# Optimization experiments

Measured on AMD Instinct MI355X. Metric: run time of the kernel, lower is better.

## Reference

```python
import jax, jax.numpy as jnp
import numpy as np

NU, NS, NV = 50000, 10000, 30000
D = 128
NUM_LAYERS = 2
EPS_US, EPS_UV, EPS_SV = 0.1, 0.1, 0.1
C_TEMP = 0.2
B = 2048


def _l2(x, eps=1e-12):
    n = jnp.sqrt(jnp.sum(x * x, axis=-1, keepdims=True))
    return x / jnp.maximum(n, eps)


def _spmm(row, col, val, x, n_out):
    # COO sparse @ dense: gather rows of x, scale, segment-reduce
    return jax.ops.segment_sum(val[:, None] * x[col], row, num_segments=n_out)


def _propagate(row, col, val, a, b, eps, key):
    feats = jnp.concatenate([a, b], axis=0)
    n = feats.shape[0]
    acc = feats  # layer-0 features are NOT normalized in the original
    for i in range(NUM_LAYERS):
        feats = _spmm(row, col, val, feats, n)
        noise = jax.random.uniform(jax.random.fold_in(key, i), feats.shape, feats.dtype)
        feats = feats + jnp.sign(feats) * _l2(noise) * eps
        acc = acc + _l2(feats)
    mean = acc / (NUM_LAYERS + 1)
    return mean[: a.shape[0]], mean[a.shape[0]:]


def _aggregate(row, col, val, x, n_out, eps, key):
    agg = _spmm(row, col, val, x, n_out)
    noise = jax.random.uniform(key, agg.shape, agg.dtype)
    return agg + jnp.sign(agg) * _l2(noise) * eps


def _mga(users_list, streamers_list, lin_w, lin_b):
    embs = [jnp.concatenate([u, s], axis=0) for u, s in zip(users_list, streamers_list)]
    query = jnp.stack(embs, axis=1)                      # (N, 3, D)
    key_e = jnp.broadcast_to(embs[0][:, None, :], query.shape)
    concat = jnp.concatenate([key_e, query], axis=2)     # (N, 3, 2D)
    logits = jnp.einsum('nkc,c->nk', concat, lin_w[0]) + lin_b[0]
    att = jax.nn.softmax(logits, axis=1)                 # (N, 3)
    out = jnp.einsum('nk,nkd->nd', att, query)
    return out[:NU], out[NU:]


def _c_loss(x):
    p = _l2(x[:, 0, :])
    pos = jnp.sum(p * p, axis=1) / C_TEMP
    ttl = jax.nn.logsumexp(p @ p.T / C_TEMP, axis=1)
    return -jnp.mean(pos - ttl)


def _forward(users_feature, streamers_feature, videos_feature, lin_w, lin_b,
             us_row, us_col, us_val, uv_row, uv_col, uv_val,
             sv_row, sv_col, sv_val,
             uv_agg_row, uv_agg_col, uv_agg_val,
             sv_agg_row, sv_agg_col, sv_agg_val, users, streamers):
    key = jax.random.key(42)
    k_us, k_uv, k_sv, k_auv, k_asv = jax.random.split(key, 5)
    US_u, US_s = _propagate(us_row, us_col, us_val, users_feature, streamers_feature, EPS_US, k_us)
    UV_u, UV_v = _propagate(uv_row, uv_col, uv_val, users_feature, videos_feature, EPS_UV, k_uv)
    UV_s = _aggregate(sv_agg_row, sv_agg_col, sv_agg_val, UV_v, NS, EPS_SV, k_asv)
    SV_s, SV_v = _propagate(sv_row, sv_col, sv_val, streamers_feature, videos_feature, EPS_SV, k_sv)
    SV_u = _aggregate(uv_agg_row, uv_agg_col, uv_agg_val, SV_v, NU, EPS_UV, k_auv)
    users_rep, streamers_rep = _mga([US_u, UV_u, SV_u], [US_s, UV_s, SV_s], lin_w, lin_b)
    s_emb = streamers_rep[streamers]                      # (B, K, D)
    u_emb = jnp.broadcast_to(users_rep[users], s_emb.shape)  # (B, K, D)
    pred = jnp.sum(u_emb * s_emb, axis=2)                 # (B, K)
    bpr = -jnp.mean(jax.nn.log_sigmoid(pred[:, :1] - pred[:, 1:]))
    c_loss = 0.5 * (_c_loss(u_emb) + _c_loss(s_emb))
    return bpr, c_loss


def setup_inputs() -> dict:
    rng = np.random.default_rng(0)

    def prop_graph(m, n, nnz):
        r = rng.integers(0, m, nnz)
        c = rng.integers(0, n, nnz)
        rows = np.concatenate([r, c + m])
        cols = np.concatenate([c + m, r])
        deg = np.bincount(rows, minlength=m + n).astype(np.float64)
        d = 1.0 / (np.sqrt(deg) + 1e-8)
        vals = (d[rows] * d[cols]).astype(np.float32)
        return rows.astype(np.int32), cols.astype(np.int32), vals, r, c

    def agg_graph(r, c, m):
        rowsum = np.bincount(r, minlength=m).astype(np.float64)
        vals = (1.0 / (rowsum + 1e-8))[r].astype(np.float32)
        return r.astype(np.int32), c.astype(np.int32), vals

    us_row, us_col, us_val, _, _ = prop_graph(NU, NS, 400000)
    uv_row, uv_col, uv_val, uv_r, uv_c = prop_graph(NU, NV, 600000)
    sv_row, sv_col, sv_val, sv_r, sv_c = prop_graph(NS, NV, 400000)
    uv_agg_row, uv_agg_col, uv_agg_val = agg_graph(uv_r, uv_c, NU)
    sv_agg_row, sv_agg_col, sv_agg_val = agg_graph(sv_r, sv_c, NS)

    key = jax.random.key(0)
    k1, k2, k3, k4, k6, k7 = jax.random.split(key, 6)
    xn = lambda k, m: jax.random.normal(k, (m, D), jnp.float32) * np.sqrt(2.0 / (m + D)).astype(np.float32)
    return {
        'users_feature': xn(k1, NU),
        'streamers_feature': xn(k2, NS),
        'videos_feature': xn(k3, NV),
        'lin_w': jax.random.uniform(k4, (1, 2 * D), jnp.float32, -1.0, 1.0) * np.sqrt(6.0 / (2 * D + 1)).astype(np.float32),
        'lin_b': jnp.zeros((1,), jnp.float32),
        'us_row': jnp.asarray(us_row), 'us_col': jnp.asarray(us_col), 'us_val': jnp.asarray(us_val),
        'uv_row': jnp.asarray(uv_row), 'uv_col': jnp.asarray(uv_col), 'uv_val': jnp.asarray(uv_val),
        'sv_row': jnp.asarray(sv_row), 'sv_col': jnp.asarray(sv_col), 'sv_val': jnp.asarray(sv_val),
        'uv_agg_row': jnp.asarray(uv_agg_row), 'uv_agg_col': jnp.asarray(uv_agg_col), 'uv_agg_val': jnp.asarray(uv_agg_val),
        'sv_agg_row': jnp.asarray(sv_agg_row), 'sv_agg_col': jnp.asarray(sv_agg_col), 'sv_agg_val': jnp.asarray(sv_agg_val),
        'users': jax.random.randint(k6, (B, 1), 0, NU, dtype=jnp.int32),
        'streamers': jax.random.randint(k7, (B, 2), 0, NS, dtype=jnp.int32),
    }


def reference(users_feature, streamers_feature, videos_feature, lin_w, lin_b,
              us_row, us_col, us_val, uv_row, uv_col, uv_val,
              sv_row, sv_col, sv_val,
              uv_agg_row, uv_agg_col, uv_agg_val,
              sv_agg_row, sv_agg_col, sv_agg_val, users, streamers):
    return _forward(users_feature, streamers_feature, videos_feature, lin_w, lin_b,
                    us_row, us_col, us_val, uv_row, uv_col, uv_val,
                    sv_row, sv_col, sv_val,
                    uv_agg_row, uv_agg_col, uv_agg_val,
                    sv_agg_row, sv_agg_col, sv_agg_val, users, streamers)
```

## Files before the change

kernel.cpp:

```cpp
#include <hip/hip_runtime.h>
#include <stdint.h>

#define D 128
constexpr int NUc = 50000, NSc = 10000, NVc = 30000, Bc = 2048;
constexpr int N_US = 60000, N_UV = 80000, N_SV = 40000, N_ALL = 90000;
constexpr int BW = 64;
constexpr int NBH = 1280;
constexpr int CHUNK = 4096;
constexpr int CAPE = 6144;

typedef _Float16 h2v __attribute__((ext_vector_type(2)));
typedef _Float16 h4v __attribute__((ext_vector_type(4)));

__host__ __device__ inline void threefry(uint32_t k0, uint32_t k1, uint32_t x0, uint32_t x1,
                                         uint32_t& o0, uint32_t& o1) {
  uint32_t ks2 = k0 ^ k1 ^ 0x1BD11BDAu;
  uint32_t v0 = x0 + k0, v1 = x1 + k1;
#define TFR(r) { v0 += v1; v1 = (v1 << (r)) | (v1 >> (32 - (r))); v1 ^= v0; }
  TFR(13) TFR(15) TFR(26) TFR(6)   v0 += k1;  v1 += ks2 + 1u;
  TFR(17) TFR(29) TFR(16) TFR(24)  v0 += ks2; v1 += k0 + 2u;
  TFR(13) TFR(15) TFR(26) TFR(6)   v0 += k0;  v1 += k1 + 3u;
  TFR(17) TFR(29) TFR(16) TFR(24)  v0 += k1;  v1 += ks2 + 4u;
  TFR(13) TFR(15) TFR(26) TFR(6)   v0 += ks2; v1 += k0 + 5u;
#undef TFR
  o0 = v0; o1 = v1;
}

__device__ __forceinline__ float unif01(uint32_t k0, uint32_t k1, uint32_t j) {
  uint32_t a, b;
  threefry(k0, k1, 0u, j, a, b);
  uint32_t bits = a ^ b;
  return __uint_as_float(0x3F800000u | (bits >> 9)) - 1.0f;
}

struct Bld {
  const int* rows[5]; const int* cols[5]; const float* vals[5];
  int* rp[5]; int* aux[5];
  int2* cv[5]; int2* ibuf[5];
  int* bhist;
  int eBase[6];
  int sBlkBase[6];
  int cBlkBase[6];
  int bktBase[6];
  int nPlus1[5];
  int thrC[5], addC[5];
};

__global__ void k_hist5(Bld b) {
  int gid = blockIdx.x * blockDim.x + threadIdx.x;
  if (gid >= b.eBase[5]) return;
  int g = 0;
  while (gid >= b.eBase[g + 1]) ++g;
  int e = gid - b.eBase[g];
  atomicAdd(&b.rp[g][b.rows[g][e] + 1], 1);
}

__global__ __launch_bounds__(1024) void k_scan1f(Bld b) {
  __shared__ int wsum[16];
  int blk = blockIdx.x;
  int g = 0;
  while (blk >= b.sBlkBase[g + 1]) ++g;
  int lb = blk - b.sBlkBase[g];
  int n = b.nPlus1[g];
  int* data = b.rp[g];
  int tid = threadIdx.x, lane = tid & 63, w = tid >> 6;
  int i = lb * 1024 + tid;
  int x = (i < n) ? data[i] : 0;
  for (int off = 1; off < 64; off <<= 1) {
    int t = __shfl_up(x, off, 64);
    if (lane >= off) x += t;
  }
  if (lane == 63) wsum[w] = x;
  __syncthreads();
  if (w == 0 && lane < 16) {
    int s = wsum[lane];
    for (int off = 1; off < 16; off <<= 1) {
      int t = __shfl_up(s, off, 64);
      if (lane >= off) s += t;
    }
    wsum[lane] = s;
  }
  __syncthreads();
  int woff = (w > 0) ? wsum[w - 1] : 0;
  if (i < n) data[i] = x + woff;
  if (tid == 1023) b.aux[g][lb] = x + woff;
}

__global__ void k_scan2f(Bld b) {
  int g = blockIdx.x;
  int nb = b.sBlkBase[g + 1] - b.sBlkBase[g];
  int* aux = b.aux[g];
  int lane = threadIdx.x;
  int carry = 0;
  for (int base = 0; base < nb; base += 64) {
    int i = base + lane;
    int v = (i < nb) ? aux[i] : 0;
    for (int off = 1; off < 64; off <<= 1) {
      int t = __shfl_up(v, off, 64);
      if (lane >= off) v += t;
    }
    if (i < nb) aux[i] = v + carry;
    carry += __shfl(v, 63, 64);
  }
}

__global__ __launch_bounds__(1024) void k_scan3f(Bld b) {
  int blk = blockIdx.x;
  int g = 0;
  while (blk >= b.sBlkBase[g + 1]) ++g;
  int lb = blk - b.sBlkBase[g];
  if (lb == 0) return;
  int i = lb * 1024 + threadIdx.x;
  if (i < b.nPlus1[g]) b.rp[g][i] += b.aux[g][lb - 1];
}

__global__ __launch_bounds__(256) void k_bhist(Bld b) {
  __shared__ int h[NBH];
  int blk = blockIdx.x;
  int g = 0;
  while (blk >= b.cBlkBase[g + 1]) ++g;
  int lblk = blk - b.cBlkBase[g];
  int nbkt = b.bktBase[g + 1] - b.bktBase[g];
  int tid = threadIdx.x;
  for (int i = tid; i < nbkt; i += 256) h[i] = 0;
  __syncthreads();
  int nnzg = b.eBase[g + 1] - b.eBase[g];
  int e0 = lblk * CHUNK;
  int eEnd = min(e0 + CHUNK, nnzg);
  for (int e = e0 + tid; e < eEnd; e += 256)
    atomicAdd(&h[b.rows[g][e] >> 6], 1);
  __syncthreads();
  int* outp = b.bhist + (size_t)blk * NBH;
  for (int i = tid; i < nbkt; i += 256) outp[i] = h[i];
}

__global__ void k_bscan(Bld b) {
  int gid = blockIdx.x * blockDim.x + threadIdx.x;
  int w = gid >> 6, lane = gid & 63;
  if (w >= b.bktBase[5]) return;
  int g = 0;
  while (w >= b.bktBase[g + 1]) ++g;
  int lb = w - b.bktBase[g];
  int carry = b.rp[g][lb * BW];
  int blk0 = b.cBlkBase[g], nblk = b.cBlkBase[g + 1] - blk0;
  for (int t = 0; t < nblk; t += 64) {
    int i = t + lane;
    int v = (i < nblk) ? b.bhist[(size_t)(blk0 + i) * NBH + lb] : 0;
    int x = v;
    for (int off = 1; off < 64; off <<= 1) {
      int tt = __shfl_up(x, off, 64);
      if (lane >= off) x += tt;
    }
    if (i < nblk) b.bhist[(size_t)(blk0 + i) * NBH + lb] = x - v + carry;
    carry += __shfl(x, 63, 64);
  }
}

__global__ __launch_bounds__(256) void k_bscat(Bld b) {
  __shared__ int cur[NBH];
  int blk = blockIdx.x;
  int g = 0;
  while (blk >= b.cBlkBase[g + 1]) ++g;
  int lblk = blk - b.cBlkBase[g];
  int nbkt = b.bktBase[g + 1] - b.bktBase[g];
  int tid = threadIdx.x;
  const int* bh = b.bhist + (size_t)blk * NBH;
  for (int i = tid; i < nbkt; i += 256) cur[i] = bh[i];
  __syncthreads();
  int nnzg = b.eBase[g + 1] - b.eBase[g];
  int e0 = lblk * CHUNK;
  int eEnd = min(e0 + CHUNK, nnzg);
  int2* ib = b.ibuf[g];
  int thr = b.thrC[g], add = b.addC[g];
  for (int e = e0 + tid; e < eEnd; e += 256) {
    int row = b.rows[g][e];
    int c = b.cols[g][e];
    c += (c >= thr) ? add : 0;
    float v = b.vals[g][e];
    uint32_t hb = (uint32_t)__builtin_bit_cast(unsigned short, (_Float16)v);
    int pos = atomicAdd(&cur[row >> 6], 1);
    ib[pos] = make_int2(c | ((row & (BW - 1)) << 17), (int)(hb | (hb << 16)));
  }
}

__global__ __launch_bounds__(256) void k_scatl2(Bld b) {
  __shared__ int lcur[BW];
  __shared__ int2 stg[CAPE];
  int bid = blockIdx.x;
  int g = 0;
  while (bid >= b.bktBase[g + 1]) ++g;
  int lb = bid - b.bktBase[g];
  int n = b.nPlus1[g] - 1;
  int r0 = lb * BW;
  int rowsInB = min(BW, n - r0);
  const int* rp = b.rp[g];
  int segStart = rp[r0];
  int segLen = rp[r0 + rowsInB] - segStart;
  int tid = threadIdx.x;
  if (tid < rowsInB) lcur[tid] = rp[r0 + tid] - segStart;
  __syncthreads();
  const int2* ib = b.ibuf[g];
  int2* cv = b.cv[g];
  for (int i = tid; i < segLen; i += 256) {
    int2 v = ib[segStart + i];
    int rowlow = ((uint32_t)v.x) >> 17;
    int2 outv = make_int2(v.x & 0x1FFFF, v.y);
    int lpos = atomicAdd(&lcur[rowlow], 1);
    if (lpos < CAPE) stg[lpos] = outv;
    else cv[segStart + lpos] = outv;
  }
  __syncthreads();
  int lim = min(segLen, CAPE);
  for (int i = tid; i < lim; i += 256) cv[segStart + i] = stg[i];
}

__global__ void k_l0(const float* __restrict__ u, const float* __restrict__ s,
                     const float* __restrict__ v, _Float16* __restrict__ L0) {
  int gid = blockIdx.x * blockDim.x + threadIdx.x;
  const int tot = N_ALL * (D / 4);
  if (gid >= tot) return;
  int r = gid >> 5, c4 = gid & 31;
  const float* src = (r < NUc) ? u + (size_t)r * D
                   : (r < NUc + NSc) ? s + (size_t)(r - NUc) * D
                                     : v + (size_t)(r - NUc - NSc) * D;
  float4 x = ((const float4*)src)[c4];
  ((h4v*)L0)[gid] = h4v{(_Float16)x.x, (_Float16)x.y, (_Float16)x.z, (_Float16)x.w};
}

__device__ __forceinline__ void gather_row(const int* __restrict__ rp,
                                           const int2* __restrict__ cv,
                                           const char* __restrict__ spc, int rl, int lane,
                                           float& fx, float& fy) {
  int s = rp[rl], e = rp[rl + 1];
  int half = lane >> 5;
  uint32_t lcol = (uint32_t)(lane & 31) << 3;
  h4v a0 = {0, 0, 0, 0}, a1 = {0, 0, 0, 0};
  int k = s;
  for (; k + 3 < e; k += 4) {
    int2 q0 = cv[k + half];
    int2 q1 = cv[k + 2 + half];
    h4v x0 = *(const h4v*)(spc + ((uint32_t)q0.x << 8) + lcol);
    h4v x1 = *(const h4v*)(spc + ((uint32_t)q1.x << 8) + lcol);
    uint2 d0 = {(uint32_t)q0.y, (uint32_t)q0.y};
    uint2 d1 = {(uint32_t)q1.y, (uint32_t)q1.y};
    a0 += x0 * __builtin_bit_cast(h4v, d0);
    a1 += x1 * __builtin_bit_cast(h4v, d1);
  }
  for (; k < e; k += 2) {
    int ke = k + half;
    int idx = (ke < e) ? ke : (e - 1);
    int2 q = cv[idx];
    uint32_t vv = (ke < e) ? (uint32_t)q.y : 0u;
    h4v x = *(const h4v*)(spc + ((uint32_t)q.x << 8) + lcol);
    uint2 dd = {vv, vv};
    a0 += x * __builtin_bit_cast(h4v, dd);
  }
  float f0 = (float)a0.x + (float)a1.x;
  float f1 = (float)a0.y + (float)a1.y;
  float f2 = (float)a0.z + (float)a1.z;
  float f3 = (float)a0.w + (float)a1.w;
  f0 += __shfl_xor(f0, 32, 64);
  f1 += __shfl_xor(f1, 32, 64);
  f2 += __shfl_xor(f2, 32, 64);
  f3 += __shfl_xor(f3, 32, 64);
  int srcl = lane >> 1;
  float v0 = __shfl(f0, srcl, 64);
  float v1 = __shfl(f1, srcl, 64);
  float v2 = __shfl(f2, srcl, 64);
  float v3 = __shfl(f3, srcl, 64);
  fx = (lane & 1) ? v2 : v0;
  fy = (lane & 1) ? v3 : v1;
}

struct GP {
  const int* rp[3]; const int2* cv[3];
  const char* src[3];
  const _Float16* accIn[3];
  _Float16* accOut[3];
  _Float16* dst[3];
  uint32_t k0[3], k1[3];
  int rowThr[3], rowAdd[3];
  int rBase[4];
  float div;
};

__global__ void k_gprop3(GP p) {
  int gid = blockIdx.x * blockDim.x + threadIdx.x;
  int r = gid >> 6, lane = gid & 63;
  if (r >= p.rBase[3]) return;
  int g = 0;
  while (r >= p.rBase[g + 1]) ++g;
  int rl = r - p.rBase[g];
  float fx, fy;
  gather_row(p.rp[g], p.cv[g], p.src[g], rl, lane, fx, fy);
  uint32_t j0 = (uint32_t)rl * D + (uint32_t)lane * 2;
  float u0 = unif01(p.k0[g], p.k1[g], j0);
  float u1 = unif01(p.k0[g], p.k1[g], j0 + 1u);
  float s2 = u0 * u0 + u1 * u1;
  for (int m = 1; m < 64; m <<= 1) s2 += __shfl_xor(s2, m, 64);
  float nn = fmaxf(sqrtf(s2), 1e-12f);
  float sg0 = (fx > 0.f) ? 1.f : ((fx < 0.f) ? -1.f : 0.f);
  float sg1 = (fy > 0.f) ? 1.f : ((fy < 0.f) ? -1.f : 0.f);
  float nf0 = fx + sg0 * (u0 / nn) * 0.1f;
  float nf1 = fy + sg1 * (u1 / nn) * 0.1f;
  float fs = nf0 * nf0 + nf1 * nf1;
  for (int m = 1; m < 64; m <<= 1) fs += __shfl_xor(fs, m, 64);
  float fn = fmaxf(sqrtf(fs), 1e-12f);
  int gr = rl + ((rl >= p.rowThr[g]) ? p.rowAdd[g] : 0);
  h2v ai = ((const h2v*)p.accIn[g])[(size_t)gr * (D / 2) + lane];
  float ax = ((float)ai.x + nf0 / fn) / p.div;
  float ay = ((float)ai.y + nf1 / fn) / p.div;
  ((h2v*)p.accOut[g])[(size_t)rl * (D / 2) + lane] = h2v{(_Float16)ax, (_Float16)ay};
  if (p.dst[g])
    ((h2v*)p.dst[g])[(size_t)gr * (D / 2) + lane] = h2v{(_Float16)nf0, (_Float16)nf1};
}

struct GA {
  const int* rp[2]; const int2* cv[2];
  const char* src[2]; _Float16* dst[2];
  uint32_t k0[2], k1[2];
  int rBase[3];
};

__global__ void k_gagg2(GA a) {
  int gid = blockIdx.x * blockDim.x + threadIdx.x;
  int r = gid >> 6, lane = gid & 63;
  if (r >= a.rBase[2]) return;
  int g = (r >= a.rBase[1]) ? 1 : 0;
  int rl = r - a.rBase[g];
  float fx, fy;
  gather_row(a.rp[g], a.cv[g], a.src[g], rl, lane, fx, fy);
  uint32_t j0 = (uint32_t)rl * D + (uint32_t)lane * 2;
  float u0 = unif01(a.k0[g], a.k1[g], j0);
  float u1 = unif01(a.k0[g], a.k1[g], j0 + 1u);
  float s2 = u0 * u0 + u1 * u1;
  for (int m = 1; m < 64; m <<= 1) s2 += __shfl_xor(s2, m, 64);
  float nn = fmaxf(sqrtf(s2), 1e-12f);
  float sg0 = (fx > 0.f) ? 1.f : ((fx < 0.f) ? -1.f : 0.f);
  float sg1 = (fy > 0.f) ? 1.f : ((fy < 0.f) ? -1.f : 0.f);
  ((h2v*)a.dst[g])[(size_t)rl * (D / 2) + lane] =
      h2v{(_Float16)(fx + sg0 * (u0 / nn) * 0.1f), (_Float16)(fy + sg1 * (u1 / nn) * 0.1f)};
}

__global__ void k_mga(_Float16* __restrict__ e0buf, const _Float16* __restrict__ UVa,
                      const _Float16* __restrict__ UVs, const _Float16* __restrict__ SVu,
                      const _Float16* __restrict__ SVa, const float* __restrict__ w,
                      const float* __restrict__ bptr) {
  int gid = blockIdx.x * blockDim.x + threadIdx.x;
  int wave = gid >> 6, lane = gid & 63;
  int n = NUc + NSc;
  if (wave >= n) return;
  const _Float16* e1 = (wave < NUc) ? UVa + (size_t)wave * D : UVs + (size_t)(wave - NUc) * D;
  const _Float16* e2 = (wave < NUc) ? SVu + (size_t)wave * D : SVa + (size_t)(wave - NUc) * D;
  _Float16* e0 = e0buf + (size_t)wave * D;
  int c = lane * 2;
  h2v h0 = *(const h2v*)(e0 + c), h1 = *(const h2v*)(e1 + c), h2_ = *(const h2v*)(e2 + c);
  float2 v0 = {(float)h0.x, (float)h0.y};
  float2 v1 = {(float)h1.x, (float)h1.y};
  float2 v2 = {(float)h2_.x, (float)h2_.y};
  float2 wl = *(const float2*)(w + c);
  float2 wh = *(const float2*)(w + D + c);
  float d00 = v0.x * wl.x + v0.y * wl.y;
  float c0 = v0.x * wh.x + v0.y * wh.y;
  float c1 = v1.x * wh.x + v1.y * wh.y;
  float c2 = v2.x * wh.x + v2.y * wh.y;
  for (int m = 1; m < 64; m <<= 1) {
    d00 += __shfl_xor(d00, m, 64);
    c0 += __shfl_xor(c0, m, 64);
    c1 += __shfl_xor(c1, m, 64);
    c2 += __shfl_xor(c2, m, 64);
  }
  float b = bptr[0];
  float l0 = d00 + c0 + b, l1 = d00 + c1 + b, l2v = d00 + c2 + b;
  float mx = fmaxf(l0, fmaxf(l1, l2v));
  float a0 = expf(l0 - mx), a1 = expf(l1 - mx), a2 = expf(l2v - mx);
  float s = a0 + a1 + a2;
  a0 /= s; a1 /= s; a2 /= s;
  float ox = a0 * v0.x + a1 * v1.x + a2 * v2.x;
  float oy = a0 * v0.y + a1 * v1.y + a2 * v2.y;
  *(h2v*)(e0 + c) = h2v{(_Float16)ox, (_Float16)oy};
}

__global__ void k_batch(const _Float16* __restrict__ reps, const int* __restrict__ users,
                        const int* __restrict__ streamers, float* __restrict__ Pu,
                        float* __restrict__ Ps, float* __restrict__ accs) {
  int gid = blockIdx.x * blockDim.x + threadIdx.x;
  int wave = gid >> 6, lane = gid & 63;
  if (wave >= Bc) return;
  int u = users[wave];
  int s0 = streamers[wave * 2], s1 = streamers[wave * 2 + 1];
  h2v uh = ((const h2v*)(reps + (size_t)u * D))[lane];
  h2v ah = ((const h2v*)(reps + (size_t)(NUc + s0) * D))[lane];
  h2v ch = ((const h2v*)(reps + (size_t)(NUc + s1) * D))[lane];
  float2 uv = {(float)uh.x, (float)uh.y};
  float2 av = {(float)ah.x, (float)ah.y};
  float2 cv = {(float)ch.x, (float)ch.y};
  float p0 = uv.x * av.x + uv.y * av.y;
  float p1 = uv.x * cv.x + uv.y * cv.y;
  float un = uv.x * uv.x + uv.y * uv.y;
  float an = av.x * av.x + av.y * av.y;
  for (int m = 1; m < 64; m <<= 1) {
    p0 += __shfl_xor(p0, m, 64);
    p1 += __shfl_xor(p1, m, 64);
    un += __shfl_xor(un, m, 64);
    an += __shfl_xor(an, m, 64);
  }
  if (lane == 0) {
    float t = p0 - p1;
    float term = fmaxf(-t, 0.f) + log1pf(expf(-fabsf(t)));
    atomicAdd(&accs[0], term);
  }
  float und = fmaxf(sqrtf(un), 1e-12f);
  float andv = fmaxf(sqrtf(an), 1e-12f);
  ((float2*)(Pu + (size_t)wave * D))[lane] = float2{uv.x / und, uv.y / und};
  ((float2*)(Ps + (size_t)wave * D))[lane] = float2{av.x / andv, av.y / andv};
}

__global__ __launch_bounds__(256) void k_cgemm(const float* __restrict__ Pu,
                                               const float* __restrict__ Ps,
                                               float* __restrict__ Su,
                                               float* __restrict__ Ss) {
  const float* P = blockIdx.z ? Ps : Pu;
  float* S = blockIdx.z ? Ss : Su;
  __shared__ float A[32][132];
  __shared__ float BT[128][68];
  int tid = threadIdx.x;
  int tx = tid & 15, ty = tid >> 4;
  int brow0 = blockIdx.x * 32;
  int j0 = blockIdx.y * 512;
#pragma unroll
  for (int i = 0; i < 4; ++i) {
    int idx = tid + i * 256;
    int r = idx >> 5, c4 = idx & 31;
    float4 v = ((const float4*)(P + (size_t)(brow0 + r) * D))[c4];
    *(float4*)&A[r][c4 * 4] = v;
  }
  float s[2] = {0.f, 0.f};
  for (int jt = 0; jt < 8; ++jt) {
    __syncthreads();
#pragma unroll
    for (int i = 0; i < 8; ++i) {
      int idx = tid + i * 256;
      int r = idx >> 5, c4 = idx & 31;
      float4 v = ((const float4*)(P + (size_t)(j0 + jt * 64 + r) * D))[c4];
      BT[c4 * 4 + 0][r] = v.x;
      BT[c4 * 4 + 1][r] = v.y;
      BT[c4 * 4 + 2][r] = v.z;
      BT[c4 * 4 + 3][r] = v.w;
    }
    __syncthreads();
    float acc[2][4] = {};
    for (int k = 0; k < 128; k += 4) {
      float4 a0 = *(const float4*)&A[ty * 2 + 0][k];
      float4 a1 = *(const float4*)&A[ty * 2 + 1][k];
      float4 b0 = *(const float4*)&BT[k + 0][tx * 4];
      float4 b1 = *(const float4*)&BT[k + 1][tx * 4];
      float4 b2 = *(const float4*)&BT[k + 2][tx * 4];
      float4 b3 = *(const float4*)&BT[k + 3][tx * 4];
      acc[0][0] = fmaf(a0.x, b0.x, acc[0][0]); acc[0][1] = fmaf(a0.x, b0.y, acc[0][1]);
      acc[0][2] = fmaf(a0.x, b0.z, acc[0][2]); acc[0][3] = fmaf(a0.x, b0.w, acc[0][3]);
      acc[1][0] = fmaf(a1.x, b0.x, acc[1][0]); acc[1][1] = fmaf(a1.x, b0.y, acc[1][1]);
      acc[1][2] = fmaf(a1.x, b0.z, acc[1][2]); acc[1][3] = fmaf(a1.x, b0.w, acc[1][3]);
      acc[0][0] = fmaf(a0.y, b1.x, acc[0][0]); acc[0][1] = fmaf(a0.y, b1.y, acc[0][1]);
      acc[0][2] = fmaf(a0.y, b1.z, acc[0][2]); acc[0][3] = fmaf(a0.y, b1.w, acc[0][3]);
      acc[1][0] = fmaf(a1.y, b1.x, acc[1][0]); acc[1][1] = fmaf(a1.y, b1.y, acc[1][1]);
      acc[1][2] = fmaf(a1.y, b1.z, acc[1][2]); acc[1][3] = fmaf(a1.y, b1.w, acc[1][3]);
      acc[0][0] = fmaf(a0.z, b2.x, acc[0][0]); acc[0][1] = fmaf(a0.z, b2.y, acc[0][1]);
      acc[0][2] = fmaf(a0.z, b2.z, acc[0][2]); acc[0][3] = fmaf(a0.z, b2.w, acc[0][3]);
      acc[1][0] = fmaf(a1.z, b2.x, acc[1][0]); acc[1][1] = fmaf(a1.z, b2.y, acc[1][1]);
      acc[1][2] = fmaf(a1.z, b2.z, acc[1][2]); acc[1][3] = fmaf(a1.z, b2.w, acc[1][3]);
      acc[0][0] = fmaf(a0.w, b3.x, acc[0][0]); acc[0][1] = fmaf(a0.w, b3.y, acc[0][1]);
      acc[0][2] = fmaf(a0.w, b3.z, acc[0][2]); acc[0][3] = fmaf(a0.w, b3.w, acc[0][3]);
      acc[1][0] = fmaf(a1.w, b3.x, acc[1][0]); acc[1][1] = fmaf(a1.w, b3.y, acc[1][1]);
      acc[1][2] = fmaf(a1.w, b3.z, acc[1][2]); acc[1][3] = fmaf(a1.w, b3.w, acc[1][3]);
    }
#pragma unroll
    for (int i = 0; i < 2; ++i)
#pragma unroll
      for (int jj = 0; jj < 4; ++jj) s[i] += __expf(5.0f * acc[i][jj]);
  }
#pragma unroll
  for (int i = 0; i < 2; ++i) {
    for (int off = 1; off < 16; off <<= 1) s[i] += __shfl_xor(s[i], off, 64);
    if (tx == 0) atomicAdd(&S[brow0 + ty * 2 + i], s[i]);
  }
}

__global__ void k_cfinal(const float* __restrict__ Pu, const float* __restrict__ Ps,
                         const float* __restrict__ Su, const float* __restrict__ Ss,
                         float* __restrict__ accs) {
  int gid = blockIdx.x * blockDim.x + threadIdx.x;
  int wave = gid >> 6, lane = gid & 63;
  if (wave >= 2 * Bc) return;
  int loss = wave >> 11, b = wave & (Bc - 1);
  const float* P = loss ? Ps : Pu;
  const float* S = loss ? Ss : Su;
  float2 p = ((const float2*)(P + (size_t)b * D))[lane];
  float pos = p.x * p.x + p.y * p.y;
  for (int m = 1; m < 64; m <<= 1) pos += __shfl_xor(pos, m, 64);
  if (lane == 0) atomicAdd(&accs[1 + loss], logf(S[b]) - 5.0f * pos);
}

__global__ void k_final(const float* __restrict__ accs, float* __restrict__ out) {
  if (threadIdx.x == 0 && blockIdx.x == 0) {
    out[0] = accs[0] / (float)Bc;
    out[1] = 0.5f * (accs[1] + accs[2]) / (float)Bc;
  }
}

extern "C" void kernel_launch(void* const* d_in, const int* in_sizes, int n_in,
                              void* d_out, int out_size, void* d_ws, size_t ws_size,
                              hipStream_t stream) {
  const float* usersF = (const float*)d_in[0];
  const float* streamersF = (const float*)d_in[1];
  const float* videosF = (const float*)d_in[2];
  const float* linW = (const float*)d_in[3];
  const float* linB = (const float*)d_in[4];
  const int* grows[5] = {(const int*)d_in[5], (const int*)d_in[8], (const int*)d_in[11],
                         (const int*)d_in[14], (const int*)d_in[17]};
  const int* gcols[5] = {(const int*)d_in[6], (const int*)d_in[9], (const int*)d_in[12],
                         (const int*)d_in[15], (const int*)d_in[18]};
  const float* gvals[5] = {(const float*)d_in[7], (const float*)d_in[10], (const float*)d_in[13],
                           (const float*)d_in[16], (const float*)d_in[19]};
  const int* users = (const int*)d_in[20];
  const int* streamers = (const int*)d_in[21];
  int nnz[5] = {in_sizes[5], in_sizes[8], in_sizes[11], in_sizes[14], in_sizes[17]};
  int gn[5] = {N_US, N_UV, N_SV, NUc, NSc};
  float* out = (float*)d_out;

  char* pb = (char*)d_ws;
  auto allocH = [&](size_t nh) { _Float16* p = (_Float16*)pb; pb += nh * 2; return p; };
  _Float16* L0 = allocH((size_t)N_ALL * D);
  _Float16* Th0 = allocH((size_t)N_US * D);
  _Float16* Th1 = allocH((size_t)N_ALL * D);
  _Float16* Th2 = allocH((size_t)N_SV * D);
  _Float16* Ac[3] = {allocH((size_t)N_US * D), allocH((size_t)N_UV * D), allocH((size_t)N_SV * D)};
  _Float16* UVsH = allocH((size_t)NSc * D);
  _Float16* SVuH = allocH((size_t)NUc * D);
  pb = (char*)(((uintptr_t)pb + 15) & ~(uintptr_t)15);
  float* Pu = (float*)pb; pb += (size_t)Bc * D * 4;
  float* Ps = (float*)pb; pb += (size_t)Bc * D * 4;
  float* accs = (float*)pb; pb += 16 * 4;
  float* Su = (float*)pb; pb += Bc * 4;
  float* Ss = (float*)pb; pb += Bc * 4;
  int totE = nnz[0] + nnz[1] + nnz[2] + nnz[3] + nnz[4];
  int2* cvAll = (int2*)pb; pb += (size_t)totE * 8;
  int2* ibAll = (int2*)pb; pb += (size_t)totE * 8;
  int* rpAll = (int*)pb;
  int totRP = 0;
  for (int g = 0; g < 5; ++g) totRP += gn[g] + 1;
  pb += (size_t)totRP * 4;
  int* auxAll = (int*)pb; pb += 5 * 128 * 4;

  Bld b;
  int totCBlk = 0;
  {
    int eA = 0, sA = 0, rpO = 0, cvO = 0, bA = 0, cA = 0;
    int thrC[5] = {0x7fffffff, NUc, 0, 0x7fffffff, 0x7fffffff};
    int addC[5] = {0, NSc, NUc, 0, 0};
    for (int g = 0; g < 5; ++g) {
      b.rows[g] = grows[g]; b.cols[g] = gcols[g]; b.vals[g] = gvals[g];
      b.thrC[g] = thrC[g]; b.addC[g] = addC[g];
      b.eBase[g] = eA; eA += nnz[g];
      int n1 = gn[g] + 1;
      b.nPlus1[g] = n1;
      b.sBlkBase[g] = sA; sA += (n1 + 1023) / 1024;
      b.cBlkBase[g] = cA; cA += (nnz[g] + CHUNK - 1) / CHUNK;
      b.rp[g] = rpAll + rpO; rpO += n1;
      b.aux[g] = auxAll + g * 128;
      b.cv[g] = cvAll + cvO;
      b.ibuf[g] = ibAll + cvO; cvO += nnz[g];
      b.bktBase[g] = bA; bA += (gn[g] + BW - 1) / BW;
    }
    b.eBase[5] = eA;
    b.sBlkBase[5] = sA;
    b.cBlkBase[5] = cA;
    b.bktBase[5] = bA;
    totCBlk = cA;
  }
  int totBlk = b.sBlkBase[5];
  int totBkt = b.bktBase[5];
  int* bhistAll = (int*)pb; pb += (size_t)totCBlk * NBH * 4;
  b.bhist = bhistAll;

  uint32_t kus[2], kuv[2], ksv[2], kauv[2], kasv[2];
  threefry(0u, 42u, 0u, 0u, kus[0], kus[1]);
  threefry(0u, 42u, 0u, 1u, kuv[0], kuv[1]);
  threefry(0u, 42u, 0u, 2u, ksv[0], ksv[1]);
  threefry(0u, 42u, 0u, 3u, kauv[0], kauv[1]);
  threefry(0u, 42u, 0u, 4u, kasv[0], kasv[1]);
  uint32_t kusL[2][2], kuvL[2][2], ksvL[2][2];
  for (uint32_t i = 0; i < 2; ++i) {
    threefry(kus[0], kus[1], 0u, i, kusL[i][0], kusL[i][1]);
    threefry(kuv[0], kuv[1], 0u, i, kuvL[i][0], kuvL[i][1]);
    threefry(ksv[0], ksv[1], 0u, i, ksvL[i][0], ksvL[i][1]);
  }

  hipMemsetAsync(rpAll, 0, (size_t)totRP * sizeof(int), stream);
  k_hist5<<<(unsigned)((totE + 255) / 256), 256, 0, stream>>>(b);
  k_scan1f<<<(unsigned)totBlk, 1024, 0, stream>>>(b);
  k_scan2f<<<5, 64, 0, stream>>>(b);
  k_scan3f<<<(unsigned)totBlk, 1024, 0, stream>>>(b);
  k_bhist<<<(unsigned)totCBlk, 256, 0, stream>>>(b);
  k_bscan<<<(unsigned)(((size_t)totBkt * 64 + 255) / 256), 256, 0, stream>>>(b);
  k_bscat<<<(unsigned)totCBlk, 256, 0, stream>>>(b);
  k_scatl2<<<(unsigned)totBkt, 256, 0, stream>>>(b);

  k_l0<<<(unsigned)((N_ALL * (D / 4) + 255) / 256), 256, 0, stream>>>(usersF, streamersF,
                                                                      videosF, L0);

  GP p1, p2;
  const uint32_t* kL1[3] = {kusL[0], kuvL[0], ksvL[0]};
  const uint32_t* kL2[3] = {kusL[1], kuvL[1], ksvL[1]};
  int rB[4] = {0, N_US, N_US + N_UV, N_US + N_UV + N_SV};
  int rThr[3] = {0x7fffffff, NUc, 0};
  int rAdd[3] = {0, NSc, NUc};
  _Float16* dstP[3] = {Th0, Th1, Th2 - (size_t)NUc * D};
  const char* src2[3] = {(const char*)Th0, (const char*)Th1,
                         (const char*)Th2 - (size_t)NUc * D * 2};
  for (int g = 0; g < 3; ++g) {
    p1.rp[g] = b.rp[g]; p1.cv[g] = b.cv[g];
    p1.src[g] = (const char*)L0; p1.accIn[g] = L0; p1.accOut[g] = Ac[g]; p1.dst[g] = dstP[g];
    p1.k0[g] = kL1[g][0]; p1.k1[g] = kL1[g][1];
    p1.rowThr[g] = rThr[g]; p1.rowAdd[g] = rAdd[g];
    p1.rBase[g] = rB[g];
    p2.rp[g] = b.rp[g]; p2.cv[g] = b.cv[g];
    p2.src[g] = src2[g]; p2.accIn[g] = Ac[g]; p2.accOut[g] = Ac[g]; p2.dst[g] = nullptr;
    p2.k0[g] = kL2[g][0]; p2.k1[g] = kL2[g][1];
    p2.rowThr[g] = 0x7fffffff; p2.rowAdd[g] = 0;
    p2.rBase[g] = rB[g];
  }
  p1.rBase[3] = rB[3]; p2.rBase[3] = rB[3];
  p1.div = 1.0f; p2.div = 3.0f;
  unsigned gpropBlocks = (unsigned)(((size_t)rB[3] * 64 + 255) / 256);
  k_gprop3<<<gpropBlocks, 256, 0, stream>>>(p1);
  k_gprop3<<<gpropBlocks, 256, 0, stream>>>(p2);

  GA ga;
  ga.rp[0] = b.rp[3]; ga.cv[0] = b.cv[3];
  ga.src[0] = (const char*)(Ac[2] + (size_t)NSc * D);
  ga.dst[0] = SVuH; ga.k0[0] = kauv[0]; ga.k1[0] = kauv[1];
  ga.rp[1] = b.rp[4]; ga.cv[1] = b.cv[4];
  ga.src[1] = (const char*)(Ac[1] + (size_t)NUc * D);
  ga.dst[1] = UVsH; ga.k0[1] = kasv[0]; ga.k1[1] = kasv[1];
  ga.rBase[0] = 0; ga.rBase[1] = NUc; ga.rBase[2] = NUc + NSc;
  k_gagg2<<<(unsigned)(((size_t)(NUc + NSc) * 64 + 255) / 256), 256, 0, stream>>>(ga);

  k_mga<<<(unsigned)((NUc + NSc + 3) / 4), 256, 0, stream>>>(Ac[0], Ac[1], UVsH, SVuH, Ac[2],
                                                             linW, linB);
  hipMemsetAsync(accs, 0, (size_t)(16 + 2 * Bc) * sizeof(float), stream);
  k_batch<<<(unsigned)((Bc + 3) / 4), 256, 0, stream>>>(Ac[0], users, streamers, Pu, Ps, accs);
  k_cgemm<<<dim3(Bc / 32, 4, 2), 256, 0, stream>>>(Pu, Ps, Su, Ss);
  k_cfinal<<<(unsigned)((2 * Bc + 3) / 4), 256, 0, stream>>>(Pu, Ps, Su, Ss, accs);
  k_final<<<1, 64, 0, stream>>>(accs, out);
}
```

Before: 897.7 us.

## Fuse row histogram, bucket histogram and L0 conversion into one kernel

```diff
diff --git a/kernel.cpp b/kernel.cpp
--- a/kernel.cpp
+++ b/kernel.cpp
@@ -46,13 +46,44 @@
   int thrC[5], addC[5];
 };
 
-__global__ void k_hist5(Bld b) {
-  int gid = blockIdx.x * blockDim.x + threadIdx.x;
-  if (gid >= b.eBase[5]) return;
+__global__ __launch_bounds__(256) void k_histl0(Bld b, const float* __restrict__ u,
+                                                const float* __restrict__ s,
+                                                const float* __restrict__ v,
+                                                _Float16* __restrict__ L0, int cBlkTot) {
+  __shared__ int h[NBH];
+  if ((int)blockIdx.x >= cBlkTot) {
+    int gid = ((int)blockIdx.x - cBlkTot) * 256 + threadIdx.x;
+    const int tot = N_ALL * (D / 4);
+    if (gid >= tot) return;
+    int r = gid >> 5, c4 = gid & 31;
+    const float* src = (r < NUc) ? u + (size_t)r * D
+                     : (r < NUc + NSc) ? s + (size_t)(r - NUc) * D
+                                       : v + (size_t)(r - NUc - NSc) * D;
+    float4 x = ((const float4*)src)[c4];
+    ((h4v*)L0)[gid] = h4v{(_Float16)x.x, (_Float16)x.y, (_Float16)x.z, (_Float16)x.w};
+    return;
+  }
+  int blk = blockIdx.x;
   int g = 0;
-  while (gid >= b.eBase[g + 1]) ++g;
-  int e = gid - b.eBase[g];
-  atomicAdd(&b.rp[g][b.rows[g][e] + 1], 1);
+  while (blk >= b.cBlkBase[g + 1]) ++g;
+  int lblk = blk - b.cBlkBase[g];
+  int nbkt = b.bktBase[g + 1] - b.bktBase[g];
+  int tid = threadIdx.x;
+  for (int i = tid; i < nbkt; i += 256) h[i] = 0;
+  __syncthreads();
+  int nnzg = b.eBase[g + 1] - b.eBase[g];
+  int e0 = lblk * CHUNK;
+  int eEnd = min(e0 + CHUNK, nnzg);
+  int* rp = b.rp[g];
+  const int* rows = b.rows[g];
+  for (int e = e0 + tid; e < eEnd; e += 256) {
+    int row = __builtin_nontemporal_load(rows + e);
+    atomicAdd(&rp[row + 1], 1);
+    atomicAdd(&h[row >> 6], 1);
+  }
+  __syncthreads();
+  int* outp = b.bhist + (size_t)blk * NBH;
+  for (int i = tid; i < nbkt; i += 256) outp[i] = h[i];
 }
 
 __global__ __launch_bounds__(1024) void k_scan1f(Bld b) {
@@ -112,26 +143,6 @@
   if (lb == 0) return;
   int i = lb * 1024 + threadIdx.x;
   if (i < b.nPlus1[g]) b.rp[g][i] += b.aux[g][lb - 1];
-}
-
-__global__ __launch_bounds__(256) void k_bhist(Bld b) {
-  __shared__ int h[NBH];
-  int blk = blockIdx.x;
-  int g = 0;
-  while (blk >= b.cBlkBase[g + 1]) ++g;
-  int lblk = blk - b.cBlkBase[g];
-  int nbkt = b.bktBase[g + 1] - b.bktBase[g];
-  int tid = threadIdx.x;
-  for (int i = tid; i < nbkt; i += 256) h[i] = 0;
-  __syncthreads();
-  int nnzg = b.eBase[g + 1] - b.eBase[g];
-  int e0 = lblk * CHUNK;
-  int eEnd = min(e0 + CHUNK, nnzg);
-  for (int e = e0 + tid; e < eEnd; e += 256)
-    atomicAdd(&h[b.rows[g][e] >> 6], 1);
-  __syncthreads();
-  int* outp = b.bhist + (size_t)blk * NBH;
-  for (int i = tid; i < nbkt; i += 256) outp[i] = h[i];
 }
 
 __global__ void k_bscan(Bld b) {
@@ -172,11 +183,14 @@
   int eEnd = min(e0 + CHUNK, nnzg);
   int2* ib = b.ibuf[g];
   int thr = b.thrC[g], add = b.addC[g];
+  const int* rows = b.rows[g];
+  const int* cols = b.cols[g];
+  const float* vals = b.vals[g];
   for (int e = e0 + tid; e < eEnd; e += 256) {
-    int row = b.rows[g][e];
-    int c = b.cols[g][e];
+    int row = __builtin_nontemporal_load(rows + e);
+    int c = __builtin_nontemporal_load(cols + e);
+    float v = __builtin_nontemporal_load(vals + e);
     c += (c >= thr) ? add : 0;
-    float v = b.vals[g][e];
     uint32_t hb = (uint32_t)__builtin_bit_cast(unsigned short, (_Float16)v);
     int pos = atomicAdd(&cur[row >> 6], 1);
     ib[pos] = make_int2(c | ((row & (BW - 1)) << 17), (int)(hb | (hb << 16)));
@@ -202,9 +216,12 @@
   const int2* ib = b.ibuf[g];
   int2* cv = b.cv[g];
   for (int i = tid; i < segLen; i += 256) {
-    int2 v = ib[segStart + i];
-    int rowlow = ((uint32_t)v.x) >> 17;
-    int2 outv = make_int2(v.x & 0x1FFFF, v.y);
+    unsigned long long raw =
+        __builtin_nontemporal_load((const unsigned long long*)(ib + segStart + i));
+    int vx = (int)(uint32_t)raw;
+    int vy = (int)(uint32_t)(raw >> 32);
+    int rowlow = ((uint32_t)vx) >> 17;
+    int2 outv = make_int2(vx & 0x1FFFF, vy);
     int lpos = atomicAdd(&lcur[rowlow], 1);
     if (lpos < CAPE) stg[lpos] = outv;
     else cv[segStart + lpos] = outv;
@@ -212,19 +229,6 @@
   __syncthreads();
   int lim = min(segLen, CAPE);
   for (int i = tid; i < lim; i += 256) cv[segStart + i] = stg[i];
-}
-
-__global__ void k_l0(const float* __restrict__ u, const float* __restrict__ s,
-                     const float* __restrict__ v, _Float16* __restrict__ L0) {
-  int gid = blockIdx.x * blockDim.x + threadIdx.x;
-  const int tot = N_ALL * (D / 4);
-  if (gid >= tot) return;
-  int r = gid >> 5, c4 = gid & 31;
-  const float* src = (r < NUc) ? u + (size_t)r * D
-                   : (r < NUc + NSc) ? s + (size_t)(r - NUc) * D
-                                     : v + (size_t)(r - NUc - NSc) * D;
-  float4 x = ((const float4*)src)[c4];
-  ((h4v*)L0)[gid] = h4v{(_Float16)x.x, (_Float16)x.y, (_Float16)x.z, (_Float16)x.w};
 }
 
 __device__ __forceinline__ void gather_row(const int* __restrict__ rp,
@@ -237,21 +241,27 @@
   h4v a0 = {0, 0, 0, 0}, a1 = {0, 0, 0, 0};
   int k = s;
   for (; k + 3 < e; k += 4) {
-    int2 q0 = cv[k + half];
-    int2 q1 = cv[k + 2 + half];
-    h4v x0 = *(const h4v*)(spc + ((uint32_t)q0.x << 8) + lcol);
-    h4v x1 = *(const h4v*)(spc + ((uint32_t)q1.x << 8) + lcol);
-    uint2 d0 = {(uint32_t)q0.y, (uint32_t)q0.y};
-    uint2 d1 = {(uint32_t)q1.y, (uint32_t)q1.y};
+    unsigned long long r0 =
+        __builtin_nontemporal_load((const unsigned long long*)(cv + k + half));
+    unsigned long long r1 =
+        __builtin_nontemporal_load((const unsigned long long*)(cv + k + 2 + half));
+    uint32_t c0 = (uint32_t)r0, c1 = (uint32_t)r1;
+    uint32_t v0 = (uint32_t)(r0 >> 32), v1 = (uint32_t)(r1 >> 32);
+    h4v x0 = *(const h4v*)(spc + (c0 << 8) + lcol);
+    h4v x1 = *(const h4v*)(spc + (c1 << 8) + lcol);
+    uint2 d0 = {v0, v0};
+    uint2 d1 = {v1, v1};
     a0 += x0 * __builtin_bit_cast(h4v, d0);
     a1 += x1 * __builtin_bit_cast(h4v, d1);
   }
   for (; k < e; k += 2) {
     int ke = k + half;
     int idx = (ke < e) ? ke : (e - 1);
-    int2 q = cv[idx];
-    uint32_t vv = (ke < e) ? (uint32_t)q.y : 0u;
-    h4v x = *(const h4v*)(spc + ((uint32_t)q.x << 8) + lcol);
+    unsigned long long r0 =
+        __builtin_nontemporal_load((const unsigned long long*)(cv + idx));
+    uint32_t cc = (uint32_t)r0;
+    uint32_t vv = (ke < e) ? (uint32_t)(r0 >> 32) : 0u;
+    h4v x = *(const h4v*)(spc + (cc << 8) + lcol);
     uint2 dd = {vv, vv};
     a0 += x * __builtin_bit_cast(h4v, dd);
   }
@@ -597,17 +607,15 @@
   }
 
   hipMemsetAsync(rpAll, 0, (size_t)totRP * sizeof(int), stream);
-  k_hist5<<<(unsigned)((totE + 255) / 256), 256, 0, stream>>>(b);
+  int l0Blocks = (N_ALL * (D / 4) + 255) / 256;
+  k_histl0<<<(unsigned)(totCBlk + l0Blocks), 256, 0, stream>>>(b, usersF, streamersF, videosF,
+                                                               L0, totCBlk);
   k_scan1f<<<(unsigned)totBlk, 1024, 0, stream>>>(b);
   k_scan2f<<<5, 64, 0, stream>>>(b);
   k_scan3f<<<(unsigned)totBlk, 1024, 0, stream>>>(b);
-  k_bhist<<<(unsigned)totCBlk, 256, 0, stream>>>(b);
   k_bscan<<<(unsigned)(((size_t)totBkt * 64 + 255) / 256), 256, 0, stream>>>(b);
   k_bscat<<<(unsigned)totCBlk, 256, 0, stream>>>(b);
   k_scatl2<<<(unsigned)totBkt, 256, 0, stream>>>(b);
-
-  k_l0<<<(unsigned)((N_ALL * (D / 4) + 255) / 256), 256, 0, stream>>>(usersF, streamersF,
-                                                                      videosF, L0);
 
   GP p1, p2;
   const uint32_t* kL1[3] = {kusL[0], kuvL[0], ksvL[0]};
```

Result: slower. 925.2 us (+3.1%).
